# Kernel tuning notes

Hardware: AMD Instinct MI355X
Metric: run time of the kernel (lower is better)

Reference implementation:

```python
import jax, jax.numpy as jnp
import numpy as np
from jax import lax

STRIDE = (1, 1)
PADDING = ((1, 1), (1, 1))
DILATION = (1, 1)


def setup_inputs() -> dict:
    key = jax.random.key(0)
    k1, k2, k3, k4 = jax.random.split(key, 4)
    bs, cin, h, w = 64, 128, 56, 56
    k_exp, cout, kh, kw = 8, 128, 3, 3
    x = jax.random.normal(k1, (bs, cin, h, w), dtype=jnp.float32)
    routing_weight = jax.random.uniform(k2, (bs, k_exp), dtype=jnp.float32)
    weight = jax.random.normal(k3, (k_exp, cout, cin, kh, kw), dtype=jnp.float32) * (1.0 / np.sqrt(cin * kh * kw))
    bias = jax.random.normal(k4, (k_exp, cout), dtype=jnp.float32) * 0.01
    return {"x": x, "routing_weight": routing_weight, "weight": weight, "bias": bias}


def reference(x, routing_weight, weight, bias):
    # CondConv combine_kernel path: per-sample kernel = routing-weighted sum of experts,
    # then a standard conv per sample (equivalent to torch groups=bs trick).
    # w_mix: [bs, oc, c, kh, kw]
    w_mix = jnp.einsum('bk,kocij->bocij', routing_weight, weight)
    b_mix = routing_weight @ bias  # [bs, oc]

    def conv_one(xi, wi):
        # xi: [c, h, w], wi: [oc, c, kh, kw]
        return lax.conv_general_dilated(
            xi[None], wi,
            window_strides=STRIDE,
            padding=PADDING,
            rhs_dilation=DILATION,
            dimension_numbers=('NCHW', 'OIHW', 'NCHW'),
        )[0]  # [oc, oh, ow]

    out = jax.vmap(conv_one)(x, w_mix)  # [bs, oc, oh, ow]
    out = out + b_mix[:, :, None, None]
    return out
```

## Files before the change

kernel.cpp:

```cpp
#include <hip/hip_runtime.h>

#define BS   64
#define CIN  128
#define OCH  128
#define HW   56
#define KEXP 8
#define KTOT 1152
#define PCOLS 58
#define PROWS 4
#define PCELLS 232
#define CPAD  68

typedef __bf16 bf16x8 __attribute__((ext_vector_type(8)));
typedef __bf16 bf16x4 __attribute__((ext_vector_type(4)));
typedef float  f32x4  __attribute__((ext_vector_type(4)));

__device__ __forceinline__ unsigned f2bf(float f) {
    union { float f; unsigned u; } v; v.f = f;
    unsigned r = v.u + 0x7fffu + ((v.u >> 16) & 1u);
    return r >> 16;
}

__device__ constexpr int KO(int s) {
    int h = s / 18, t = s - h * 18;
    return (t >> 1) * 128 + h * 64 + (t & 1) * 32;
}

__global__ __launch_bounds__(256) void prep_wmix(
        const float* __restrict__ rw, const float* __restrict__ wgt,
        unsigned short* __restrict__ wmix) {
    __shared__ float wlds[KEXP * KTOT];
    __shared__ float rwl[16 * KEXP];
    int oc  = blockIdx.x;
    int bg  = blockIdx.y;
    int tid = threadIdx.x;

    if (tid < 16 * KEXP) rwl[tid] = rw[bg * 16 * KEXP + tid];
    const float* wsrc = wgt + (size_t)oc * KTOT;
    #pragma unroll
    for (int e = 0; e < KEXP; ++e) {
        const float* we = wsrc + (size_t)e * OCH * KTOT;
        for (int j = tid; j < KTOT; j += 256) wlds[e * KTOT + j] = we[j];
    }
    __syncthreads();

    for (int t = tid; t < KTOT; t += 256) {
        int c = t & 127, rs = t >> 7;
        float w8[KEXP];
        #pragma unroll
        for (int e = 0; e < KEXP; ++e) w8[e] = wlds[e * KTOT + c * 9 + rs];
        #pragma unroll
        for (int b = 0; b < 16; ++b) {
            float a = 0.f;
            #pragma unroll
            for (int e = 0; e < KEXP; ++e) a += rwl[b * KEXP + e] * w8[e];
            wmix[((size_t)(bg * 16 + b) * OCH + oc) * KTOT + t] = (unsigned short)f2bf(a);
        }
    }
}

__global__ __launch_bounds__(256) void prep_bmix(
        const float* __restrict__ rw, const float* __restrict__ bias,
        float* __restrict__ bmix) {
    int i = blockIdx.x * 256 + threadIdx.x;
    int b = i >> 7, oc = i & 127;
    float a = 0.f;
    #pragma unroll
    for (int e = 0; e < KEXP; ++e) a += rw[b * KEXP + e] * bias[e * OCH + oc];
    bmix[i] = a;
}

__global__ __launch_bounds__(256, 4) void condconv_mfma(
        const float* __restrict__ x, const unsigned short* __restrict__ wmix,
        const float* __restrict__ bmix, float* __restrict__ out) {
    __shared__ unsigned short patch[PCELLS * CPAD];

    int blk  = blockIdx.x;
    int b    = blk & 63;
    int tile = blk >> 6;
    int oh0  = tile * 2;
    int tid  = threadIdx.x;
    int wave = tid >> 6, lane = tid & 63, ln = lane & 15, quad = lane >> 4;

    const unsigned short* wmb = wmix + (size_t)b * OCH * KTOT;
    const unsigned short* a0p = wmb + (size_t)(wave * 32 + ln) * KTOT + quad * 8;
    const unsigned short* a1p = a0p + (size_t)16 * KTOT;

    bf16x8 pa0[2], pa1[2];
    pa0[0] = *(const bf16x8*)(a0p + KO(0));
    pa1[0] = *(const bf16x8*)(a1p + KO(0));
    pa0[1] = *(const bf16x8*)(a0p + KO(1));
    pa1[1] = *(const bf16x8*)(a1p + KO(1));

    const float* xb = x + (size_t)b * CIN * HW * HW;
    auto stage = [&](int h) {
        const float* xh = xb + (size_t)h * 64 * HW * HW;
        #pragma unroll 4
        for (int it = 0; it < 16; ++it) {
            int i   = it * 256 + tid;
            int col = i & 63;
            int y   = (i >> 6) & 3;
            int cq  = i >> 8;
            if (col < PCOLS) {
                int ih = oh0 + y - 1, iw = col - 1;
                float v0 = 0.f, v1 = 0.f, v2 = 0.f, v3 = 0.f;
                if ((unsigned)ih < 56u && (unsigned)iw < 56u) {
                    const float* r0 = xh + ((size_t)(cq * 4) * HW + ih) * HW + iw;
                    v0 = r0[0];
                    v1 = r0[HW * HW];
                    v2 = r0[2 * HW * HW];
                    v3 = r0[3 * HW * HW];
                }
                unsigned p0 = f2bf(v0) | (f2bf(v1) << 16);
                unsigned p1 = f2bf(v2) | (f2bf(v3) << 16);
                int cell = y * PCOLS + col;
                *(uint2*)&patch[cell * CPAD + cq * 4] = make_uint2(p0, p1);
            }
        }
    };

    int cbq[7], offn[7];
    #pragma unroll
    for (int nt = 0; nt < 7; ++nt) {
        int n   = nt * 16 + ln;
        int row = (n >= 56) ? 1 : 0;
        int ow  = n - row * 56;
        cbq[nt]  = (row * PCOLS + ow) * CPAD + quad * 8;
        offn[nt] = (oh0 + row) * HW + ow;
    }

    f32x4 acc[2][7] = {};

    stage(0);
    __syncthreads();
    #pragma unroll
    for (int t = 0; t < 18; ++t) {
        bf16x8 ca0 = pa0[t & 1], ca1 = pa1[t & 1];
        pa0[t & 1] = *(const bf16x8*)(a0p + KO(t + 2));
        pa1[t & 1] = *(const bf16x8*)(a1p + KO(t + 2));
        const int rs = t >> 1, cc = t & 1;
        const int r = rs / 3, sc = rs - r * 3;
        const int pshift = (r * PCOLS + sc) * CPAD + cc * 32;
        #pragma unroll
        for (int nt = 0; nt < 7; ++nt) {
            int boff = cbq[nt] + pshift;
            bf16x4 lo = *(const bf16x4*)&patch[boff];
            bf16x4 hi = *(const bf16x4*)&patch[boff + 4];
            bf16x8 bb = __builtin_shufflevector(lo, hi, 0, 1, 2, 3, 4, 5, 6, 7);
            acc[0][nt] = __builtin_amdgcn_mfma_f32_16x16x32_bf16(ca0, bb, acc[0][nt], 0, 0, 0);
            acc[1][nt] = __builtin_amdgcn_mfma_f32_16x16x32_bf16(ca1, bb, acc[1][nt], 0, 0, 0);
        }
    }
    __syncthreads();
    stage(1);
    __syncthreads();
    #pragma unroll
    for (int t = 18; t < 36; ++t) {
        bf16x8 ca0 = pa0[t & 1], ca1 = pa1[t & 1];
        if (t < 34) {
            pa0[t & 1] = *(const bf16x8*)(a0p + KO(t + 2));
            pa1[t & 1] = *(const bf16x8*)(a1p + KO(t + 2));
        }
        const int tt = t - 18;
        const int rs = tt >> 1, cc = tt & 1;
        const int r = rs / 3, sc = rs - r * 3;
        const int pshift = (r * PCOLS + sc) * CPAD + cc * 32;
        #pragma unroll
        for (int nt = 0; nt < 7; ++nt) {
            int boff = cbq[nt] + pshift;
            bf16x4 lo = *(const bf16x4*)&patch[boff];
            bf16x4 hi = *(const bf16x4*)&patch[boff + 4];
            bf16x8 bb = __builtin_shufflevector(lo, hi, 0, 1, 2, 3, 4, 5, 6, 7);
            acc[0][nt] = __builtin_amdgcn_mfma_f32_16x16x32_bf16(ca0, bb, acc[0][nt], 0, 0, 0);
            acc[1][nt] = __builtin_amdgcn_mfma_f32_16x16x32_bf16(ca1, bb, acc[1][nt], 0, 0, 0);
        }
    }

    const float* bmb = bmix + b * OCH;
    float* ob = out + (size_t)b * OCH * HW * HW;
    #pragma unroll
    for (int mt = 0; mt < 2; ++mt) {
        #pragma unroll
        for (int rg = 0; rg < 4; ++rg) {
            int oc = wave * 32 + mt * 16 + quad * 4 + rg;
            float bv = bmb[oc];
            #pragma unroll
            for (int nt = 0; nt < 7; ++nt)
                ob[(size_t)oc * (HW * HW) + offn[nt]] = acc[mt][nt][rg] + bv;
        }
    }
}

extern "C" void kernel_launch(void* const* d_in, const int* in_sizes, int n_in,
                              void* d_out, int out_size, void* d_ws, size_t ws_size,
                              hipStream_t stream) {
    (void)in_sizes; (void)n_in; (void)out_size; (void)ws_size;
    const float* x    = (const float*)d_in[0];
    const float* rw   = (const float*)d_in[1];
    const float* wgt  = (const float*)d_in[2];
    const float* bias = (const float*)d_in[3];
    float* outp = (float*)d_out;

    unsigned short* wmix = (unsigned short*)d_ws;
    float* bmix = (float*)((char*)d_ws + (size_t)BS * OCH * KTOT * 2);

    hipLaunchKernelGGL(prep_wmix, dim3(OCH, 4), dim3(256), 0, stream, rw, wgt, wmix);
    hipLaunchKernelGGL(prep_bmix, dim3(32), dim3(256), 0, stream, rw, bias, bmix);
    hipLaunchKernelGGL(condconv_mfma, dim3(BS * 28), dim3(256), 0, stream,
                       x, wmix, bmix, outp);
}
```

Before: 292.9 us.

## Pre-convert input to padded bf16 channel-blocked layout and stream via global_load_lds

Adds a prep kernel that converts x to bf16 in a zero-padded, channel-quad-blocked layout (40-element cells, including spatial border padding). The main conv kernel then copies contiguous slabs into double-buffered LDS with async global-to-LDS loads, overlapping the next channel block's load with MFMA work. The mixed weights are also relaid out so that per-step A fragments are contiguous. This removes the per-block fp32 load and conversion and the strided gathers. In exchange it adds an extra pass over x in HBM, with its own write and read.

```diff
diff --git a/kernel.cpp b/kernel.cpp
--- a/kernel.cpp
+++ b/kernel.cpp
@@ -1,18 +1,20 @@
 #include <hip/hip_runtime.h>
 
-#define BS   64
-#define CIN  128
-#define OCH  128
-#define HW   56
-#define KEXP 8
-#define KTOT 1152
-#define PCOLS 58
-#define PROWS 4
-#define PCELLS 232
-#define CPAD  68
+#define BS    64
+#define CIN   128
+#define OCH   128
+#define HW    56
+#define KEXP  8
+#define KTOT  1152
+#define NSTEP 36
+#define CELLE 40
+#define ROWE  (58 * CELLE)
+#define PLANEE (58 * ROWE)
+#define WMIX_PS (NSTEP * OCH * 32)
+#define SLAB_CHUNKS 1160
+#define BUFE 10240
 
 typedef __bf16 bf16x8 __attribute__((ext_vector_type(8)));
-typedef __bf16 bf16x4 __attribute__((ext_vector_type(4)));
 typedef float  f32x4  __attribute__((ext_vector_type(4)));
 
 __device__ __forceinline__ unsigned f2bf(float f) {
@@ -21,9 +23,42 @@
     return r >> 16;
 }
 
-__device__ constexpr int KO(int s) {
-    int h = s / 18, t = s - h * 18;
-    return (t >> 1) * 128 + h * 64 + (t & 1) * 32;
+__device__ __forceinline__ void gl16(const unsigned short* g, unsigned short* l) {
+    __builtin_amdgcn_global_load_lds(
+        (const __attribute__((address_space(1))) void*)g,
+        (__attribute__((address_space(3))) void*)l, 16, 0, 0);
+}
+
+__global__ __launch_bounds__(256) void prep_xt(const float* __restrict__ x,
+                                               unsigned short* __restrict__ xt) {
+    __shared__ unsigned short t[CIN * HW];
+    int b = blockIdx.x, ihp = blockIdx.y;
+    int tid = threadIdx.x;
+    bool border = (ihp == 0) || (ihp == 57);
+    if (!border) {
+        int ih = ihp - 1;
+        const float* xr = x + (size_t)b * CIN * HW * HW + (size_t)ih * HW;
+        for (int i = tid; i < CIN * 28; i += 256) {
+            int c = i / 28, w2 = i - c * 28;
+            float2 v = *(const float2*)(xr + (size_t)c * (HW * HW) + w2 * 2);
+            unsigned pk = f2bf(v.x) | (f2bf(v.y) << 16);
+            *(unsigned*)&t[c * HW + w2 * 2] = pk;
+        }
+    }
+    __syncthreads();
+    for (int j = tid; j < 4 * 58 * 5; j += 256) {
+        int q = j / 290, rr = j - q * 290;
+        int cell = rr / 5, p = rr - cell * 5;
+        union { unsigned short u[8]; uint4 v; } o;
+        o.v = make_uint4(0u, 0u, 0u, 0u);
+        if (!border && p < 4 && cell >= 1 && cell <= 56) {
+            #pragma unroll
+            for (int k = 0; k < 8; ++k)
+                o.u[k] = t[(q * 32 + p * 8 + k) * HW + (cell - 1)];
+        }
+        *(uint4*)&xt[((size_t)(b * 4 + q) * 3364 + (size_t)ihp * 58) * CELLE
+                     + cell * CELLE + p * 8] = o.v;
+    }
 }
 
 __global__ __launch_bounds__(256) void prep_wmix(
@@ -46,6 +81,8 @@
 
     for (int t = tid; t < KTOT; t += 256) {
         int c = t & 127, rs = t >> 7;
+        int q = c >> 5, cl = c & 31;
+        size_t oidx = ((size_t)(q * 9 + rs) * OCH + oc) * 32 + cl;
         float w8[KEXP];
         #pragma unroll
         for (int e = 0; e < KEXP; ++e) w8[e] = wlds[e * KTOT + c * 9 + rs];
@@ -54,7 +91,7 @@
             float a = 0.f;
             #pragma unroll
             for (int e = 0; e < KEXP; ++e) a += rwl[b * KEXP + e] * w8[e];
-            wmix[((size_t)(bg * 16 + b) * OCH + oc) * KTOT + t] = (unsigned short)f2bf(a);
+            wmix[(size_t)(bg * 16 + b) * WMIX_PS + oidx] = (unsigned short)f2bf(a);
         }
     }
 }
@@ -71,9 +108,9 @@
 }
 
 __global__ __launch_bounds__(256, 4) void condconv_mfma(
-        const float* __restrict__ x, const unsigned short* __restrict__ wmix,
+        const unsigned short* __restrict__ xt, const unsigned short* __restrict__ wmix,
         const float* __restrict__ bmix, float* __restrict__ out) {
-    __shared__ unsigned short patch[PCELLS * CPAD];
+    __shared__ unsigned short patch[2][BUFE];
 
     int blk  = blockIdx.x;
     int b    = blk & 63;
@@ -82,98 +119,65 @@
     int tid  = threadIdx.x;
     int wave = tid >> 6, lane = tid & 63, ln = lane & 15, quad = lane >> 4;
 
-    const unsigned short* wmb = wmix + (size_t)b * OCH * KTOT;
-    const unsigned short* a0p = wmb + (size_t)(wave * 32 + ln) * KTOT + quad * 8;
-    const unsigned short* a1p = a0p + (size_t)16 * KTOT;
-
-    bf16x8 pa0[2], pa1[2];
-    pa0[0] = *(const bf16x8*)(a0p + KO(0));
-    pa1[0] = *(const bf16x8*)(a1p + KO(0));
-    pa0[1] = *(const bf16x8*)(a0p + KO(1));
-    pa1[1] = *(const bf16x8*)(a1p + KO(1));
-
-    const float* xb = x + (size_t)b * CIN * HW * HW;
-    auto stage = [&](int h) {
-        const float* xh = xb + (size_t)h * 64 * HW * HW;
-        #pragma unroll 4
-        for (int it = 0; it < 16; ++it) {
-            int i   = it * 256 + tid;
-            int col = i & 63;
-            int y   = (i >> 6) & 3;
-            int cq  = i >> 8;
-            if (col < PCOLS) {
-                int ih = oh0 + y - 1, iw = col - 1;
-                float v0 = 0.f, v1 = 0.f, v2 = 0.f, v3 = 0.f;
-                if ((unsigned)ih < 56u && (unsigned)iw < 56u) {
-                    const float* r0 = xh + ((size_t)(cq * 4) * HW + ih) * HW + iw;
-                    v0 = r0[0];
-                    v1 = r0[HW * HW];
-                    v2 = r0[2 * HW * HW];
-                    v3 = r0[3 * HW * HW];
-                }
-                unsigned p0 = f2bf(v0) | (f2bf(v1) << 16);
-                unsigned p1 = f2bf(v2) | (f2bf(v3) << 16);
-                int cell = y * PCOLS + col;
-                *(uint2*)&patch[cell * CPAD + cq * 4] = make_uint2(p0, p1);
-            }
-        }
-    };
-
-    int cbq[7], offn[7];
+    const unsigned short* ap = wmix + (size_t)b * WMIX_PS
+                             + (size_t)(wave * 32 + ln) * 32 + quad * 8;
+
+    const unsigned short* xbase = xt + (size_t)(b * 4) * PLANEE + (size_t)oh0 * ROWE;
+    int g[5];
+    #pragma unroll
+    for (int i = 0; i < 5; ++i) {
+        int gi = wave * 320 + i * 64 + lane;
+        g[i] = (gi < SLAB_CHUNKS) ? gi : (SLAB_CHUNKS - 1);
+    }
+
+    int cb[7], offn[7];
     #pragma unroll
     for (int nt = 0; nt < 7; ++nt) {
         int n   = nt * 16 + ln;
         int row = (n >= 56) ? 1 : 0;
         int ow  = n - row * 56;
-        cbq[nt]  = (row * PCOLS + ow) * CPAD + quad * 8;
+        cb[nt]   = (row * 58 + ow) * CELLE + quad * 8;
         offn[nt] = (oh0 + row) * HW + ow;
     }
 
     f32x4 acc[2][7] = {};
 
-    stage(0);
+    auto stage = [&](int q, int bf) {
+        const unsigned short* sq = xbase + (size_t)q * PLANEE;
+        unsigned short* l0 = &patch[bf][0] + wave * 2560;
+        #pragma unroll
+        for (int i = 0; i < 5; ++i)
+            gl16(sq + (size_t)g[i] * 8, l0 + i * 512);
+    };
+
+    stage(0, 0);
+    bf16x8 pa0[2], pa1[2];
+    pa0[0] = *(const bf16x8*)(ap);
+    pa1[0] = *(const bf16x8*)(ap + 512);
+    pa0[1] = *(const bf16x8*)(ap + 4096);
+    pa1[1] = *(const bf16x8*)(ap + 4096 + 512);
     __syncthreads();
-    #pragma unroll
-    for (int t = 0; t < 18; ++t) {
-        bf16x8 ca0 = pa0[t & 1], ca1 = pa1[t & 1];
-        pa0[t & 1] = *(const bf16x8*)(a0p + KO(t + 2));
-        pa1[t & 1] = *(const bf16x8*)(a1p + KO(t + 2));
-        const int rs = t >> 1, cc = t & 1;
-        const int r = rs / 3, sc = rs - r * 3;
-        const int pshift = (r * PCOLS + sc) * CPAD + cc * 32;
-        #pragma unroll
-        for (int nt = 0; nt < 7; ++nt) {
-            int boff = cbq[nt] + pshift;
-            bf16x4 lo = *(const bf16x4*)&patch[boff];
-            bf16x4 hi = *(const bf16x4*)&patch[boff + 4];
-            bf16x8 bb = __builtin_shufflevector(lo, hi, 0, 1, 2, 3, 4, 5, 6, 7);
-            acc[0][nt] = __builtin_amdgcn_mfma_f32_16x16x32_bf16(ca0, bb, acc[0][nt], 0, 0, 0);
-            acc[1][nt] = __builtin_amdgcn_mfma_f32_16x16x32_bf16(ca1, bb, acc[1][nt], 0, 0, 0);
-        }
-    }
-    __syncthreads();
-    stage(1);
-    __syncthreads();
-    #pragma unroll
-    for (int t = 18; t < 36; ++t) {
-        bf16x8 ca0 = pa0[t & 1], ca1 = pa1[t & 1];
-        if (t < 34) {
-            pa0[t & 1] = *(const bf16x8*)(a0p + KO(t + 2));
-            pa1[t & 1] = *(const bf16x8*)(a1p + KO(t + 2));
-        }
-        const int tt = t - 18;
-        const int rs = tt >> 1, cc = tt & 1;
-        const int r = rs / 3, sc = rs - r * 3;
-        const int pshift = (r * PCOLS + sc) * CPAD + cc * 32;
-        #pragma unroll
-        for (int nt = 0; nt < 7; ++nt) {
-            int boff = cbq[nt] + pshift;
-            bf16x4 lo = *(const bf16x4*)&patch[boff];
-            bf16x4 hi = *(const bf16x4*)&patch[boff + 4];
-            bf16x8 bb = __builtin_shufflevector(lo, hi, 0, 1, 2, 3, 4, 5, 6, 7);
-            acc[0][nt] = __builtin_amdgcn_mfma_f32_16x16x32_bf16(ca0, bb, acc[0][nt], 0, 0, 0);
-            acc[1][nt] = __builtin_amdgcn_mfma_f32_16x16x32_bf16(ca1, bb, acc[1][nt], 0, 0, 0);
-        }
+
+    #pragma unroll
+    for (int q = 0; q < 4; ++q) {
+        if (q < 3) stage(q + 1, (q + 1) & 1);
+        #pragma unroll
+        for (int s9 = 0; s9 < 9; ++s9) {
+            const int s = q * 9 + s9;
+            bf16x8 ca0 = pa0[s & 1], ca1 = pa1[s & 1];
+            const int sp = (s + 2 < NSTEP) ? (s + 2) : (NSTEP - 1);
+            pa0[s & 1] = *(const bf16x8*)(ap + (size_t)sp * 4096);
+            pa1[s & 1] = *(const bf16x8*)(ap + (size_t)sp * 4096 + 512);
+            const int r = s9 / 3, sc = s9 - r * 3;
+            const int pshift = (r * 58 + sc) * CELLE;
+            #pragma unroll
+            for (int nt = 0; nt < 7; ++nt) {
+                bf16x8 bb = *(const bf16x8*)&patch[q & 1][cb[nt] + pshift];
+                acc[0][nt] = __builtin_amdgcn_mfma_f32_16x16x32_bf16(ca0, bb, acc[0][nt], 0, 0, 0);
+                acc[1][nt] = __builtin_amdgcn_mfma_f32_16x16x32_bf16(ca1, bb, acc[1][nt], 0, 0, 0);
+            }
+        }
+        __syncthreads();
     }
 
     const float* bmb = bmix + b * OCH;
@@ -202,10 +206,12 @@
     float* outp = (float*)d_out;
 
     unsigned short* wmix = (unsigned short*)d_ws;
-    float* bmix = (float*)((char*)d_ws + (size_t)BS * OCH * KTOT * 2);
-
+    float* bmix = (float*)((char*)d_ws + (size_t)BS * WMIX_PS * 2);
+    unsigned short* xtw = (unsigned short*)((char*)d_ws + (size_t)BS * WMIX_PS * 2 + 32768);
+
+    hipLaunchKernelGGL(prep_xt,   dim3(BS, 58), dim3(256), 0, stream, x, xtw);
     hipLaunchKernelGGL(prep_wmix, dim3(OCH, 4), dim3(256), 0, stream, rw, wgt, wmix);
-    hipLaunchKernelGGL(prep_bmix, dim3(32), dim3(256), 0, stream, rw, bias, bmix);
+    hipLaunchKernelGGL(prep_bmix, dim3(32),     dim3(256), 0, stream, rw, bias, bmix);
     hipLaunchKernelGGL(condconv_mfma, dim3(BS * 28), dim3(256), 0, stream,
-                       x, wmix, bmix, outp);
-}
+                       xtw, wmix, bmix, outp);
+}
```

After: 274.9 us. 6.2% less time.
